# Performance work log

Measured on AMD Instinct MI355X. Metric: run time of the kernel, lower is better.

## Reference

```python
import jax, jax.numpy as jnp
import numpy as np

TOPK = 180          # init kwarg topk
TOL = 3             # init kwarg tolerance_px


def setup_inputs() -> dict:
    key = jax.random.key(0)
    k1, k2, k3 = jax.random.split(key, 3)
    shape = (32, 1, 512, 512)
    return {
        "rv": jax.random.normal(k1, shape, dtype=jnp.float32),
        "ri": jax.random.normal(k2, shape, dtype=jnp.float32),
        "rf": jax.random.normal(k3, shape, dtype=jnp.float32),
    }


def reference(rv, ri, rf):
    # rf already matches rv spatially, so the interpolate branch is a no-op.
    b, c, h, w = rv.shape
    n = c * h * w
    rv_flat = rv.reshape(b, n)
    ri_flat = ri.reshape(b, n)
    rf_flat = rf.reshape(b, n)

    k = min(TOPK, n)
    _, rv_idx = jax.lax.top_k(rv_flat, k)                 # [b, k]
    _, ri_idx = jax.lax.top_k(ri_flat, k)                 # [b, k]
    _, rf_idx = jax.lax.top_k(rf_flat, min(2 * k, n))     # [b, 2k]

    rows = jnp.arange(b)[:, None]
    # union mask of VIS+IR keypoints (scatter 1.0 at top-k indices)
    src_mask = (
        jnp.zeros((b, n), jnp.float32)
        .at[rows, rv_idx].set(1.0)
        .at[rows, ri_idx].set(1.0)
    )
    src_mask = (src_mask > 0).astype(jnp.float32).reshape(b, c, h, w)

    fused_mask = (
        jnp.zeros((b, n), jnp.float32).at[rows, rf_idx].set(1.0)
    ).reshape(b, c, h, w)

    if TOL > 0:
        ksz = 2 * TOL + 1
        # max_pool2d(kernel=ksz, stride=1, padding=TOL) == dilation of the mask
        fused_mask = jax.lax.reduce_window(
            fused_mask, -jnp.inf, jax.lax.max,
            window_dimensions=(1, 1, ksz, ksz),
            window_strides=(1, 1, 1, 1),
            padding=[(0, 0), (0, 0), (TOL, TOL), (TOL, TOL)],
        )

    fused_hit = (fused_mask > 0).astype(jnp.float32)
    cover = (src_mask * fused_hit).reshape(b, -1).sum(axis=1)
    denom = jnp.maximum(src_mask.reshape(b, -1).sum(axis=1), 1.0)
    coverage = cover / denom
    return (1.0 - coverage).mean()
```

## Files before the change

### kernel.cpp

```cpp
#include <hip/hip_runtime.h>

#define N_ELEM 262144
#define SPLIT 32
#define NTS 256
#define CAPG_MAX 8192
#define LCAP 2048
#define TIE_CAP 512
#define THRESH 2.5f

__device__ __forceinline__ unsigned keyOf(float f) {
    unsigned u = __float_as_uint(f);
    return (u & 0x80000000u) ? ~u : (u | 0x80000000u);
}

__device__ __forceinline__ const float* pairSrc(int p, const float* rv, const float* ri, const float* rf) {
    int t = p % 3, b = p / 3;
    return (t == 0 ? rv : (t == 1 ? ri : rf)) + (size_t)b * N_ELEM;
}

__global__ void zero_kernel(int* __restrict__ cnt, int P, float* __restrict__ out) {
    int i = threadIdx.x + blockIdx.x * blockDim.x;
    if (i < P) cnt[i] = 0;
    if (i == 0) *out = 0.0f;
}

__global__ __launch_bounds__(NTS) void collect_kernel(const float* __restrict__ rv,
                                                      const float* __restrict__ ri,
                                                      const float* __restrict__ rf,
                                                      int* __restrict__ cnt,
                                                      unsigned long long* __restrict__ cand,
                                                      int capg) {
    const int p = blockIdx.x / SPLIT;
    const int s = blockIdx.x % SPLIT;
    const float4* p4 = (const float4*)pairSrc(p, rv, ri, rf) + (size_t)s * (N_ELEM / 4 / SPLIT);

    __shared__ unsigned long long buf[LCAP];
    __shared__ int s_m, s_base;
    const int tid = threadIdx.x;
    if (tid == 0) s_m = 0;
    __syncthreads();

    const int base_idx = s * (N_ELEM / SPLIT);
    for (int i = tid; i < N_ELEM / 4 / SPLIT; i += NTS) {
        float4 v = p4[i];
        int pos;
        if (v.x > THRESH) { pos = atomicAdd(&s_m, 1); if (pos < LCAP) buf[pos] = ((unsigned long long)keyOf(v.x) << 32) | (unsigned)(base_idx + 4 * i + 0); }
        if (v.y > THRESH) { pos = atomicAdd(&s_m, 1); if (pos < LCAP) buf[pos] = ((unsigned long long)keyOf(v.y) << 32) | (unsigned)(base_idx + 4 * i + 1); }
        if (v.z > THRESH) { pos = atomicAdd(&s_m, 1); if (pos < LCAP) buf[pos] = ((unsigned long long)keyOf(v.z) << 32) | (unsigned)(base_idx + 4 * i + 2); }
        if (v.w > THRESH) { pos = atomicAdd(&s_m, 1); if (pos < LCAP) buf[pos] = ((unsigned long long)keyOf(v.w) << 32) | (unsigned)(base_idx + 4 * i + 3); }
    }
    __syncthreads();

    int m = s_m;
    const bool over = (m > LCAP);
    if (over) m = LCAP;
    if (tid == 0) {
        int add = over ? (m + capg + 1) : m;
        s_base = atomicAdd(&cnt[p], add);
    }
    __syncthreads();

    const int base = s_base;
    unsigned long long* mycand = cand + (size_t)p * capg;
    for (int i = tid; i < m; i += NTS) {
        int pos = base + i;
        if (pos < capg) mycand[pos] = buf[i];
    }
}

__global__ __launch_bounds__(NTS) void select_kernel(const float* __restrict__ rv,
                                                     const float* __restrict__ ri,
                                                     const float* __restrict__ rf,
                                                     const int* __restrict__ cnt,
                                                     const unsigned long long* __restrict__ cand,
                                                     int capg,
                                                     int* __restrict__ idx_out) {
    const int p = blockIdx.x;
    const int t = p % 3;
    const int K = (t == 2) ? 360 : 180;
    int* obuf = idx_out + (size_t)p * 360;
    const unsigned long long* mycand = cand + (size_t)p * capg;
    const float4* p4 = (const float4*)pairSrc(p, rv, ri, rf);

    __shared__ unsigned suf[257];
    __shared__ int ties[TIE_CAP];
    __shared__ unsigned s_p2; __shared__ int s_b2; __shared__ int s_cg2;
    __shared__ int s_on; __shared__ int s_tn;
    const int tid = threadIdx.x;

    const int cn = cnt[p];
    const bool fits = (cn >= K) && (cn <= capg);

    if (tid == 0) { s_p2 = 0; s_b2 = 0; s_cg2 = 0; }
    __syncthreads();

    while (s_b2 < 32) {
        if (tid < 256) suf[tid] = 0;
        __syncthreads();
        {
            const int b2 = s_b2; const unsigned p2 = s_p2;
            const int sh2 = 24 - b2;
            if (fits) {
                for (int i = tid; i < cn; i += NTS) {
                    unsigned kk = (unsigned)(mycand[i] >> 32);
                    bool match = (b2 == 0) || ((kk >> (32 - b2)) == p2);
                    if (match) atomicAdd(&suf[(kk >> sh2) & 255u], 1u);
                }
            } else {
                for (int i = tid; i < N_ELEM / 4; i += NTS) {
                    float4 v = p4[i];
                    unsigned kk;
                    kk = keyOf(v.x); if ((b2 == 0) || ((kk >> (32 - b2)) == p2)) atomicAdd(&suf[(kk >> sh2) & 255u], 1u);
                    kk = keyOf(v.y); if ((b2 == 0) || ((kk >> (32 - b2)) == p2)) atomicAdd(&suf[(kk >> sh2) & 255u], 1u);
                    kk = keyOf(v.z); if ((b2 == 0) || ((kk >> (32 - b2)) == p2)) atomicAdd(&suf[(kk >> sh2) & 255u], 1u);
                    kk = keyOf(v.w); if ((b2 == 0) || ((kk >> (32 - b2)) == p2)) atomicAdd(&suf[(kk >> sh2) & 255u], 1u);
                }
            }
        }
        __syncthreads();
        for (int off = 1; off < 256; off <<= 1) {
            unsigned add = (tid < 256 && tid + off < 256) ? suf[tid + off] : 0u;
            __syncthreads();
            if (tid < 256) suf[tid] += add;
            __syncthreads();
        }
        {
            const unsigned r = (unsigned)(K - s_cg2);
            __syncthreads();
            if (tid < 256) {
                unsigned below = (tid == 255) ? 0u : suf[tid + 1];
                if (suf[tid] >= r && below < r) {
                    s_p2 = (s_p2 << 8) | (unsigned)tid;
                    s_b2 += 8;
                    s_cg2 += (int)below;
                }
            }
        }
        __syncthreads();
    }

    if (tid == 0) { s_on = 0; s_tn = 0; }
    __syncthreads();

    {
        const unsigned Kth = s_p2;
        if (fits) {
            for (int i = tid; i < cn; i += NTS) {
                unsigned long long e = mycand[i];
                unsigned kk = (unsigned)(e >> 32);
                int idx = (int)(e & 0xffffffffu);
                if (kk > Kth) { int pos = atomicAdd(&s_on, 1); obuf[pos] = idx; }
                else if (kk == Kth) { int pos = atomicAdd(&s_tn, 1); if (pos < TIE_CAP) ties[pos] = idx; }
            }
        } else {
            for (int i = tid; i < N_ELEM / 4; i += NTS) {
                float4 v = p4[i];
                float vals[4] = {v.x, v.y, v.z, v.w};
                for (int c = 0; c < 4; ++c) {
                    unsigned kk = keyOf(vals[c]);
                    if (kk > Kth) { int pos = atomicAdd(&s_on, 1); obuf[pos] = 4 * i + c; }
                    else if (kk == Kth) { int pos = atomicAdd(&s_tn, 1); if (pos < TIE_CAP) ties[pos] = 4 * i + c; }
                }
            }
        }
    }
    __syncthreads();
    if (tid == 0) {
        int need = K - s_cg2;
        int tn = s_tn; if (tn > TIE_CAP) tn = TIE_CAP;
        int rr = need; if (rr > tn) rr = tn;
        for (int a = 0; a < rr; ++a) {
            int mb = a;
            for (int j = a + 1; j < tn; ++j) if (ties[j] < ties[mb]) mb = j;
            int tmp = ties[a]; ties[a] = ties[mb]; ties[mb] = tmp;
            obuf[s_on + a] = ties[a];
        }
        for (int a = rr; a < need; ++a) obuf[s_on + a] = (tn > 0) ? ties[0] : 0;
    }
}

__global__ __launch_bounds__(256) void coverage_kernel(const int* __restrict__ idx_buf,
                                                       float* __restrict__ out,
                                                       float inv_b) {
    const int b = blockIdx.x;
    __shared__ int cnd[360];
    __shared__ int fy[360];
    __shared__ int fx[360];
    __shared__ int s_u, s_c;
    const int* rvI = idx_buf + (size_t)(b * 3 + 0) * 360;
    const int* riI = idx_buf + (size_t)(b * 3 + 1) * 360;
    const int* rfI = idx_buf + (size_t)(b * 3 + 2) * 360;
    const int tid = threadIdx.x;

    for (int i = tid; i < 180; i += blockDim.x) { cnd[i] = rvI[i]; cnd[180 + i] = riI[i]; }
    for (int i = tid; i < 360; i += blockDim.x) { int v = rfI[i]; fy[i] = v >> 9; fx[i] = v & 511; }
    if (tid == 0) { s_u = 0; s_c = 0; }
    __syncthreads();

    int myu = 0, myc = 0;
    for (int i = tid; i < 360; i += blockDim.x) {
        const int v = cnd[i];
        const int y = v >> 9, x = v & 511;
        int dup = 0;
        #pragma unroll 8
        for (int j = 0; j < 360; ++j) dup |= (int)((j < i) & (cnd[j] == v));
        int cov = 0;
        #pragma unroll 8
        for (int j = 0; j < 360; ++j) {
            int dy = y - fy[j]; dy = (dy < 0) ? -dy : dy;
            int dx = x - fx[j]; dx = (dx < 0) ? -dx : dx;
            cov |= (int)((dy <= 3) & (dx <= 3));
        }
        if (!dup) { myu += 1; myc += cov; }
    }
    if (myu) atomicAdd(&s_u, myu);
    if (myc) atomicAdd(&s_c, myc);
    __syncthreads();
    if (tid == 0) {
        float denom = (float)(s_u > 0 ? s_u : 1);
        float loss = 1.0f - (float)s_c / denom;
        atomicAdd(out, loss * inv_b);
    }
}

extern "C" void kernel_launch(void* const* d_in, const int* in_sizes, int n_in,
                              void* d_out, int out_size, void* d_ws, size_t ws_size,
                              hipStream_t stream) {
    const float* rv = (const float*)d_in[0];
    const float* ri = (const float*)d_in[1];
    const float* rf = (const float*)d_in[2];
    float* out = (float*)d_out;

    const int B = in_sizes[0] / N_ELEM;
    const int P = 3 * B;

    char* ws = (char*)d_ws;
    int* cnt = (int*)ws;
    int* idx_buf = (int*)(ws + (size_t)P * 4);
    size_t fixed = (size_t)P * 4 + (size_t)P * 360 * 4;
    fixed = (fixed + 7) & ~(size_t)7;
    unsigned long long* cand = (unsigned long long*)(ws + fixed);
    size_t avail = (ws_size > fixed) ? (ws_size - fixed) / ((size_t)P * 8) : 0;
    int capg = (int)(avail < CAPG_MAX ? avail : CAPG_MAX);

    zero_kernel<<<1, 256, 0, stream>>>(cnt, P, out);
    collect_kernel<<<P * SPLIT, NTS, 0, stream>>>(rv, ri, rf, cnt, cand, capg);
    select_kernel<<<P, NTS, 0, stream>>>(rv, ri, rf, cnt, cand, capg, idx_buf);
    coverage_kernel<<<B, 256, 0, stream>>>(idx_buf, out, 1.0f / (float)B);
}
```

Measured before the change: 175.2 us.

## Fuse zero/select/coverage kernels and use per-slice candidate buckets staged in LDS

Drops the separate zero kernel by having block 0 of collect initialise the output and per-batch done counters. Each collect block now writes its candidates to a fixed per-slice bucket with no global atomics, and select prefix-sums the slice counts with wave shuffles and copies the candidates into shared memory. The radix pick step uses a single-wave shuffle suffix scan in place of the multi-sync shared scan. Coverage is folded into the select kernel through a last-block-done counter, removing two launches in exchange for threadfence and atomic-counter synchronisation.

```diff
diff --git a/kernel.cpp b/kernel.cpp
--- a/kernel.cpp
+++ b/kernel.cpp
@@ -3,8 +3,8 @@
 #define N_ELEM 262144
 #define SPLIT 32
 #define NTS 256
-#define CAPG_MAX 8192
-#define LCAP 2048
+#define SLICE_CAP 256
+#define LSEL 2048
 #define TIE_CAP 512
 #define THRESH 2.5f
 
@@ -18,25 +18,25 @@
     return (t == 0 ? rv : (t == 1 ? ri : rf)) + (size_t)b * N_ELEM;
 }
 
-__global__ void zero_kernel(int* __restrict__ cnt, int P, float* __restrict__ out) {
-    int i = threadIdx.x + blockIdx.x * blockDim.x;
-    if (i < P) cnt[i] = 0;
-    if (i == 0) *out = 0.0f;
-}
-
 __global__ __launch_bounds__(NTS) void collect_kernel(const float* __restrict__ rv,
                                                       const float* __restrict__ ri,
                                                       const float* __restrict__ rf,
-                                                      int* __restrict__ cnt,
+                                                      int* __restrict__ cntS,
                                                       unsigned long long* __restrict__ cand,
-                                                      int capg) {
+                                                      float* __restrict__ out,
+                                                      int* __restrict__ done, int B) {
     const int p = blockIdx.x / SPLIT;
     const int s = blockIdx.x % SPLIT;
     const float4* p4 = (const float4*)pairSrc(p, rv, ri, rf) + (size_t)s * (N_ELEM / 4 / SPLIT);
 
-    __shared__ unsigned long long buf[LCAP];
-    __shared__ int s_m, s_base;
+    __shared__ unsigned long long buf[SLICE_CAP];
+    __shared__ int s_m;
     const int tid = threadIdx.x;
+
+    if (blockIdx.x == 0) {
+        if (tid < B) done[tid] = 0;
+        if (tid == B) *out = 0.0f;
+    }
     if (tid == 0) s_m = 0;
     __syncthreads();
 
@@ -44,97 +44,128 @@
     for (int i = tid; i < N_ELEM / 4 / SPLIT; i += NTS) {
         float4 v = p4[i];
         int pos;
-        if (v.x > THRESH) { pos = atomicAdd(&s_m, 1); if (pos < LCAP) buf[pos] = ((unsigned long long)keyOf(v.x) << 32) | (unsigned)(base_idx + 4 * i + 0); }
-        if (v.y > THRESH) { pos = atomicAdd(&s_m, 1); if (pos < LCAP) buf[pos] = ((unsigned long long)keyOf(v.y) << 32) | (unsigned)(base_idx + 4 * i + 1); }
-        if (v.z > THRESH) { pos = atomicAdd(&s_m, 1); if (pos < LCAP) buf[pos] = ((unsigned long long)keyOf(v.z) << 32) | (unsigned)(base_idx + 4 * i + 2); }
-        if (v.w > THRESH) { pos = atomicAdd(&s_m, 1); if (pos < LCAP) buf[pos] = ((unsigned long long)keyOf(v.w) << 32) | (unsigned)(base_idx + 4 * i + 3); }
+        if (v.x > THRESH) { pos = atomicAdd(&s_m, 1); if (pos < SLICE_CAP) buf[pos] = ((unsigned long long)keyOf(v.x) << 32) | (unsigned)(base_idx + 4 * i + 0); }
+        if (v.y > THRESH) { pos = atomicAdd(&s_m, 1); if (pos < SLICE_CAP) buf[pos] = ((unsigned long long)keyOf(v.y) << 32) | (unsigned)(base_idx + 4 * i + 1); }
+        if (v.z > THRESH) { pos = atomicAdd(&s_m, 1); if (pos < SLICE_CAP) buf[pos] = ((unsigned long long)keyOf(v.z) << 32) | (unsigned)(base_idx + 4 * i + 2); }
+        if (v.w > THRESH) { pos = atomicAdd(&s_m, 1); if (pos < SLICE_CAP) buf[pos] = ((unsigned long long)keyOf(v.w) << 32) | (unsigned)(base_idx + 4 * i + 3); }
     }
     __syncthreads();
 
     int m = s_m;
-    const bool over = (m > LCAP);
-    if (over) m = LCAP;
-    if (tid == 0) {
-        int add = over ? (m + capg + 1) : m;
-        s_base = atomicAdd(&cnt[p], add);
-    }
-    __syncthreads();
-
-    const int base = s_base;
-    unsigned long long* mycand = cand + (size_t)p * capg;
-    for (int i = tid; i < m; i += NTS) {
-        int pos = base + i;
-        if (pos < capg) mycand[pos] = buf[i];
-    }
-}
-
-__global__ __launch_bounds__(NTS) void select_kernel(const float* __restrict__ rv,
-                                                     const float* __restrict__ ri,
-                                                     const float* __restrict__ rf,
-                                                     const int* __restrict__ cnt,
-                                                     const unsigned long long* __restrict__ cand,
-                                                     int capg,
-                                                     int* __restrict__ idx_out) {
+    const bool over = (m > SLICE_CAP);
+    if (over) m = SLICE_CAP;
+    if (tid == 0) cntS[p * SPLIT + s] = over ? -1 : m;
+    unsigned long long* my = cand + (size_t)(p * SPLIT + s) * SLICE_CAP;
+    for (int i = tid; i < m; i += NTS) my[i] = buf[i];
+}
+
+__global__ __launch_bounds__(NTS) void select_cov_kernel(const float* __restrict__ rv,
+                                                         const float* __restrict__ ri,
+                                                         const float* __restrict__ rf,
+                                                         const int* __restrict__ cntS,
+                                                         const unsigned long long* __restrict__ cand,
+                                                         int* __restrict__ idx_out,
+                                                         int* __restrict__ done,
+                                                         float* __restrict__ out,
+                                                         float inv_b) {
     const int p = blockIdx.x;
     const int t = p % 3;
+    const int bb = p / 3;
     const int K = (t == 2) ? 360 : 180;
     int* obuf = idx_out + (size_t)p * 360;
-    const unsigned long long* mycand = cand + (size_t)p * capg;
+    const int tid = threadIdx.x;
+
+    __shared__ unsigned long long lc[LSEL];
+    __shared__ unsigned hist[256];
+    __shared__ int ties[TIE_CAP];
+    __shared__ int soff[SPLIT]; __shared__ int scnt[SPLIT];
+    __shared__ int s_total, s_bad;
+    __shared__ unsigned s_p2; __shared__ int s_b2; __shared__ int s_cg2;
+    __shared__ int s_on, s_tn, s_pickd; __shared__ unsigned s_pickb;
+    __shared__ int s_prev;
+
+    if (tid < 64) {
+        int c = (tid < SPLIT) ? cntS[p * SPLIT + tid] : 0;
+        int bad = (c < 0) ? 1 : 0;
+        int cc = bad ? 0 : c;
+        int v = cc;
+        #pragma unroll
+        for (int off = 1; off < 64; off <<= 1) {
+            int u = __shfl_up(v, off, 64);
+            if (tid >= off) v += u;
+        }
+        if (tid < SPLIT) { soff[tid] = v - cc; scnt[tid] = cc; }
+        if (tid == 63) s_total = v;
+        unsigned long long bm = __ballot(bad != 0);
+        if (tid == 0) s_bad = (bm != 0ull) ? 1 : 0;
+    }
+    __syncthreads();
+    const int total = s_total;
+    const bool fits = (!s_bad) && (total >= K) && (total <= LSEL);
+
+    if (fits) {
+        const int sl = tid >> 3;
+        const int j0 = tid & 7;
+        const unsigned long long* src = cand + (size_t)(p * SPLIT + sl) * SLICE_CAP;
+        const int c = scnt[sl];
+        const int o = soff[sl];
+        for (int j = j0; j < c; j += 8) lc[o + j] = src[j];
+    }
+    __syncthreads();
+
     const float4* p4 = (const float4*)pairSrc(p, rv, ri, rf);
 
-    __shared__ unsigned suf[257];
-    __shared__ int ties[TIE_CAP];
-    __shared__ unsigned s_p2; __shared__ int s_b2; __shared__ int s_cg2;
-    __shared__ int s_on; __shared__ int s_tn;
-    const int tid = threadIdx.x;
-
-    const int cn = cnt[p];
-    const bool fits = (cn >= K) && (cn <= capg);
-
     if (tid == 0) { s_p2 = 0; s_b2 = 0; s_cg2 = 0; }
     __syncthreads();
 
     while (s_b2 < 32) {
-        if (tid < 256) suf[tid] = 0;
+        hist[tid] = 0;
         __syncthreads();
         {
             const int b2 = s_b2; const unsigned p2 = s_p2;
             const int sh2 = 24 - b2;
             if (fits) {
-                for (int i = tid; i < cn; i += NTS) {
-                    unsigned kk = (unsigned)(mycand[i] >> 32);
+                for (int i = tid; i < total; i += NTS) {
+                    unsigned kk = (unsigned)(lc[i] >> 32);
                     bool match = (b2 == 0) || ((kk >> (32 - b2)) == p2);
-                    if (match) atomicAdd(&suf[(kk >> sh2) & 255u], 1u);
+                    if (match) atomicAdd(&hist[(kk >> sh2) & 255u], 1u);
                 }
             } else {
                 for (int i = tid; i < N_ELEM / 4; i += NTS) {
                     float4 v = p4[i];
                     unsigned kk;
-                    kk = keyOf(v.x); if ((b2 == 0) || ((kk >> (32 - b2)) == p2)) atomicAdd(&suf[(kk >> sh2) & 255u], 1u);
-                    kk = keyOf(v.y); if ((b2 == 0) || ((kk >> (32 - b2)) == p2)) atomicAdd(&suf[(kk >> sh2) & 255u], 1u);
-                    kk = keyOf(v.z); if ((b2 == 0) || ((kk >> (32 - b2)) == p2)) atomicAdd(&suf[(kk >> sh2) & 255u], 1u);
-                    kk = keyOf(v.w); if ((b2 == 0) || ((kk >> (32 - b2)) == p2)) atomicAdd(&suf[(kk >> sh2) & 255u], 1u);
+                    kk = keyOf(v.x); if ((b2 == 0) || ((kk >> (32 - b2)) == p2)) atomicAdd(&hist[(kk >> sh2) & 255u], 1u);
+                    kk = keyOf(v.y); if ((b2 == 0) || ((kk >> (32 - b2)) == p2)) atomicAdd(&hist[(kk >> sh2) & 255u], 1u);
+                    kk = keyOf(v.z); if ((b2 == 0) || ((kk >> (32 - b2)) == p2)) atomicAdd(&hist[(kk >> sh2) & 255u], 1u);
+                    kk = keyOf(v.w); if ((b2 == 0) || ((kk >> (32 - b2)) == p2)) atomicAdd(&hist[(kk >> sh2) & 255u], 1u);
                 }
             }
         }
         __syncthreads();
-        for (int off = 1; off < 256; off <<= 1) {
-            unsigned add = (tid < 256 && tid + off < 256) ? suf[tid + off] : 0u;
-            __syncthreads();
-            if (tid < 256) suf[tid] += add;
-            __syncthreads();
-        }
-        {
-            const unsigned r = (unsigned)(K - s_cg2);
-            __syncthreads();
-            if (tid < 256) {
-                unsigned below = (tid == 255) ? 0u : suf[tid + 1];
-                if (suf[tid] >= r && below < r) {
-                    s_p2 = (s_p2 << 8) | (unsigned)tid;
-                    s_b2 += 8;
-                    s_cg2 += (int)below;
-                }
-            }
+        const unsigned r = (unsigned)(K - s_cg2);
+        if (tid < 64) {
+            const int l = tid;
+            unsigned h0 = hist[4*l+0], h1 = hist[4*l+1], h2 = hist[4*l+2], h3 = hist[4*l+3];
+            unsigned sum4 = h0 + h1 + h2 + h3;
+            unsigned suf = sum4;
+            #pragma unroll
+            for (int off = 1; off < 64; off <<= 1) {
+                unsigned u = __shfl_down(suf, off, 64);
+                if (l + off < 64) suf += u;
+            }
+            unsigned s0 = suf, s1 = s0 - h0, s2 = s1 - h1, s3 = s2 - h2, s4 = s3 - h3;
+            int d = -1; unsigned below = 0;
+            if      (s3 >= r && s4 < r) { d = 4*l+3; below = s4; }
+            else if (s2 >= r && s3 < r) { d = 4*l+2; below = s3; }
+            else if (s1 >= r && s2 < r) { d = 4*l+1; below = s2; }
+            else if (s0 >= r && s1 < r) { d = 4*l+0; below = s1; }
+            if (d >= 0) { s_pickd = d; s_pickb = below; }
+        }
+        __syncthreads();
+        if (tid == 0) {
+            s_p2 = (s_p2 << 8) | (unsigned)s_pickd;
+            s_cg2 += (int)s_pickb;
+            s_b2 += 8;
         }
         __syncthreads();
     }
@@ -145,8 +176,8 @@
     {
         const unsigned Kth = s_p2;
         if (fits) {
-            for (int i = tid; i < cn; i += NTS) {
-                unsigned long long e = mycand[i];
+            for (int i = tid; i < total; i += NTS) {
+                unsigned long long e = lc[i];
                 unsigned kk = (unsigned)(e >> 32);
                 int idx = (int)(e & 0xffffffffu);
                 if (kk > Kth) { int pos = atomicAdd(&s_on, 1); obuf[pos] = idx; }
@@ -177,49 +208,47 @@
         }
         for (int a = rr; a < need; ++a) obuf[s_on + a] = (tn > 0) ? ties[0] : 0;
     }
-}
-
-__global__ __launch_bounds__(256) void coverage_kernel(const int* __restrict__ idx_buf,
-                                                       float* __restrict__ out,
-                                                       float inv_b) {
-    const int b = blockIdx.x;
-    __shared__ int cnd[360];
-    __shared__ int fy[360];
-    __shared__ int fx[360];
-    __shared__ int s_u, s_c;
-    const int* rvI = idx_buf + (size_t)(b * 3 + 0) * 360;
-    const int* riI = idx_buf + (size_t)(b * 3 + 1) * 360;
-    const int* rfI = idx_buf + (size_t)(b * 3 + 2) * 360;
-    const int tid = threadIdx.x;
-
-    for (int i = tid; i < 180; i += blockDim.x) { cnd[i] = rvI[i]; cnd[180 + i] = riI[i]; }
-    for (int i = tid; i < 360; i += blockDim.x) { int v = rfI[i]; fy[i] = v >> 9; fx[i] = v & 511; }
-    if (tid == 0) { s_u = 0; s_c = 0; }
-    __syncthreads();
-
-    int myu = 0, myc = 0;
-    for (int i = tid; i < 360; i += blockDim.x) {
-        const int v = cnd[i];
-        const int y = v >> 9, x = v & 511;
-        int dup = 0;
-        #pragma unroll 8
-        for (int j = 0; j < 360; ++j) dup |= (int)((j < i) & (cnd[j] == v));
-        int cov = 0;
-        #pragma unroll 8
-        for (int j = 0; j < 360; ++j) {
-            int dy = y - fy[j]; dy = (dy < 0) ? -dy : dy;
-            int dx = x - fx[j]; dx = (dx < 0) ? -dx : dx;
-            cov |= (int)((dy <= 3) & (dx <= 3));
-        }
-        if (!dup) { myu += 1; myc += cov; }
-    }
-    if (myu) atomicAdd(&s_u, myu);
-    if (myc) atomicAdd(&s_c, myc);
-    __syncthreads();
-    if (tid == 0) {
-        float denom = (float)(s_u > 0 ? s_u : 1);
-        float loss = 1.0f - (float)s_c / denom;
-        atomicAdd(out, loss * inv_b);
+
+    __threadfence();
+    __syncthreads();
+    if (tid == 0) s_prev = atomicAdd(&done[bb], 1);
+    __syncthreads();
+    if (s_prev == 2) {
+        __threadfence();
+        __shared__ int cnd[360]; __shared__ int fy[360]; __shared__ int fx[360];
+        __shared__ int s_u, s_c;
+        const int* rvI = idx_out + (size_t)(bb * 3 + 0) * 360;
+        const int* riI = idx_out + (size_t)(bb * 3 + 1) * 360;
+        const int* rfI = idx_out + (size_t)(bb * 3 + 2) * 360;
+        for (int i = tid; i < 180; i += NTS) { cnd[i] = rvI[i]; cnd[180 + i] = riI[i]; }
+        for (int i = tid; i < 360; i += NTS) { int v = rfI[i]; fy[i] = v >> 9; fx[i] = v & 511; }
+        if (tid == 0) { s_u = 0; s_c = 0; }
+        __syncthreads();
+
+        int myu = 0, myc = 0;
+        for (int i = tid; i < 360; i += NTS) {
+            const int v = cnd[i];
+            const int y = v >> 9, x = v & 511;
+            int dup = 0;
+            #pragma unroll 8
+            for (int j = 0; j < 360; ++j) dup |= (int)((j < i) & (cnd[j] == v));
+            int cov = 0;
+            #pragma unroll 8
+            for (int j = 0; j < 360; ++j) {
+                int dy = y - fy[j]; dy = (dy < 0) ? -dy : dy;
+                int dx = x - fx[j]; dx = (dx < 0) ? -dx : dx;
+                cov |= (int)((dy <= 3) & (dx <= 3));
+            }
+            if (!dup) { myu += 1; myc += cov; }
+        }
+        if (myu) atomicAdd(&s_u, myu);
+        if (myc) atomicAdd(&s_c, myc);
+        __syncthreads();
+        if (tid == 0) {
+            float denom = (float)(s_u > 0 ? s_u : 1);
+            float loss = 1.0f - (float)s_c / denom;
+            atomicAdd(out, loss * inv_b);
+        }
     }
 }
 
@@ -235,16 +264,13 @@
     const int P = 3 * B;
 
     char* ws = (char*)d_ws;
-    int* cnt = (int*)ws;
-    int* idx_buf = (int*)(ws + (size_t)P * 4);
-    size_t fixed = (size_t)P * 4 + (size_t)P * 360 * 4;
+    int* cntS = (int*)ws;
+    int* done = (int*)(ws + (size_t)P * SPLIT * 4);
+    int* idx_buf = (int*)(ws + (size_t)P * SPLIT * 4 + (size_t)B * 4);
+    size_t fixed = (size_t)P * SPLIT * 4 + (size_t)B * 4 + (size_t)P * 360 * 4;
     fixed = (fixed + 7) & ~(size_t)7;
     unsigned long long* cand = (unsigned long long*)(ws + fixed);
-    size_t avail = (ws_size > fixed) ? (ws_size - fixed) / ((size_t)P * 8) : 0;
-    int capg = (int)(avail < CAPG_MAX ? avail : CAPG_MAX);
-
-    zero_kernel<<<1, 256, 0, stream>>>(cnt, P, out);
-    collect_kernel<<<P * SPLIT, NTS, 0, stream>>>(rv, ri, rf, cnt, cand, capg);
-    select_kernel<<<P, NTS, 0, stream>>>(rv, ri, rf, cnt, cand, capg, idx_buf);
-    coverage_kernel<<<B, 256, 0, stream>>>(idx_buf, out, 1.0f / (float)B);
-}
+
+    collect_kernel<<<P * SPLIT, NTS, 0, stream>>>(rv, ri, rf, cntS, cand, out, done, B);
+    select_cov_kernel<<<P, NTS, 0, stream>>>(rv, ri, rf, cntS, cand, idx_buf, done, out, 1.0f / (float)B);
+}
```

After: 170.3 us. 2.8% less time.
